# Optimization experiments

Hardware: AMD Instinct MI355X
Metric: run time of the kernel (lower is better)

## Reference

```python
import jax, jax.numpy as jnp
import numpy as np

D_MODEL = 1024
N_HEADS = 16
HEAD_DIM = D_MODEL // N_HEADS


def setup_inputs() -> dict:
    key = jax.random.key(0)
    k_x, k_wqkv, k_bqkv, k_wo, k_bo = jax.random.split(key, 5)
    b, t = 4, 2048
    s = 1.0 / np.sqrt(D_MODEL)
    return {
        "x": jax.random.normal(k_x, (b, t, D_MODEL), dtype=jnp.float32),
        "w_qkv": jax.random.uniform(k_wqkv, (D_MODEL, 3 * D_MODEL), jnp.float32, -s, s),
        "b_qkv": jax.random.uniform(k_bqkv, (3 * D_MODEL,), jnp.float32, -s, s),
        "w_out": jax.random.uniform(k_wo, (D_MODEL, D_MODEL), jnp.float32, -s, s),
        "b_out": jax.random.uniform(k_bo, (D_MODEL,), jnp.float32, -s, s),
    }


def reference(x, w_qkv, b_qkv, w_out, b_out):
    b, t, _ = x.shape
    # fused QKV projection -> [b, t, 3, h, d] -> q,k,v each [b, h, t, d]
    qkv = (x @ w_qkv + b_qkv).reshape(b, t, 3, N_HEADS, HEAD_DIM)
    q, k, v = jnp.moveaxis(qkv, 2, 0)          # each [b, t, h, d]
    q = q.transpose(0, 2, 1, 3)                # [b, h, t, d]
    k = k.transpose(0, 2, 1, 3)
    v = v.transpose(0, 2, 1, 3)
    scale = 1.0 / np.sqrt(HEAD_DIM).astype(np.float32)
    logits = jnp.einsum('bhqd,bhkd->bhqk', q, k) * scale
    causal = jnp.tril(jnp.ones((t, t), dtype=bool))
    logits = jnp.where(causal, logits, jnp.finfo(logits.dtype).min)
    attn = jax.nn.softmax(logits, axis=-1)
    out = jnp.einsum('bhqk,bhkd->bhqd', attn, v)      # [b, h, t, d]
    out = out.transpose(0, 2, 1, 3).reshape(b, t, D_MODEL)
    return out @ w_out + b_out
```

## Files before the change

### kernel.cpp

```cpp
#include <hip/hip_runtime.h>
#include <hip/hip_bf16.h>
#include <math.h>

#define NHEADS 16
#define HDIM   64
#define SEQT   2048
#define NBATCH 4
#define DMODEL 1024
#define MROWS  (NBATCH * SEQT)

typedef __bf16 bf16;
typedef bf16  bf16x8 __attribute__((ext_vector_type(8)));
typedef float f32x4  __attribute__((ext_vector_type(4)));
typedef float f32x16 __attribute__((ext_vector_type(16)));
typedef unsigned int u32x4 __attribute__((ext_vector_type(4)));

#define MFMA_BF16(a, b, c) __builtin_amdgcn_mfma_f32_16x16x32_bf16((a), (b), (c), 0, 0, 0)
#define MFMA32(a, b, c)    __builtin_amdgcn_mfma_f32_32x32x16_bf16((a), (b), (c), 0, 0, 0)
#define Z16 {0.f,0.f,0.f,0.f,0.f,0.f,0.f,0.f,0.f,0.f,0.f,0.f,0.f,0.f,0.f,0.f}
#define LOG2E 1.44269504f

__device__ __forceinline__ void gload_lds16(const void* g, void* l) {
  __builtin_amdgcn_global_load_lds((const __attribute__((address_space(1))) void*)g,
                                   (__attribute__((address_space(3))) void*)l, 16, 0, 0);
}

__device__ __forceinline__ unsigned cvtpk_bf16(float lo, float hi) {
  unsigned r;
  asm("v_cvt_pk_bf16_f32 %0, %1, %2" : "=v"(r) : "v"(lo), "v"(hi));
  return r;
}
__device__ __forceinline__ void plswap(unsigned& a, unsigned& b) {
  asm volatile("v_permlane32_swap_b32 %0, %1" : "+v"(a), "+v"(b));
}
__device__ __forceinline__ float exp2v(float x) {
  float r;
  asm("v_exp_f32 %0, %1" : "=v"(r) : "v"(x));
  return r;
}


__global__ __launch_bounds__(256) void k_cvt_f32_bf16(const float* __restrict__ in,
                                                      bf16* __restrict__ out, int n8) {
  int i = blockIdx.x * blockDim.x + threadIdx.x;
  if (i >= n8) return;
  const float4* in4 = (const float4*)in;
  float4 a = in4[(size_t)i * 2], b = in4[(size_t)i * 2 + 1];
  bf16x8 v;
  v[0] = (bf16)a.x; v[1] = (bf16)a.y; v[2] = (bf16)a.z; v[3] = (bf16)a.w;
  v[4] = (bf16)b.x; v[5] = (bf16)b.y; v[6] = (bf16)b.z; v[7] = (bf16)b.w;
  *(bf16x8*)(out + (size_t)i * 8) = v;
}

__global__ __launch_bounds__(256) void k_transpose_f32_bf16(const float* __restrict__ in,
                                                            bf16* __restrict__ out,
                                                            int R, int C) {
  int nct = C >> 6;
  int rt = blockIdx.x / nct, ct = blockIdx.x % nct;
  __shared__ float tile[64][65];
  int tid = threadIdx.x;
#pragma unroll
  for (int i = 0; i < 16; i++) {
    int e = i * 256 + tid, r = e >> 6, c = e & 63;
    tile[r][c] = in[(size_t)(rt * 64 + r) * C + ct * 64 + c];
  }
  __syncthreads();
#pragma unroll
  for (int i = 0; i < 16; i++) {
    int e = i * 256 + tid, r = e >> 6, c = e & 63;
    out[(size_t)(ct * 64 + r) * R + rt * 64 + c] = (bf16)tile[c][r];
  }
}

__global__ __launch_bounds__(256) void k_transpose_v(const bf16* __restrict__ v,
                                                     bf16* __restrict__ vt) {
  int tt = blockIdx.x & 31;
  int bh = blockIdx.x >> 5;
  __shared__ bf16 tile[64][65];
  int tid = threadIdx.x;
  const bf16* src = v + (size_t)bh * SEQT * 64 + (size_t)tt * 64 * 64;
#pragma unroll
  for (int i = 0; i < 16; i++) {
    int e = i * 256 + tid, r = e >> 6, c = e & 63;
    tile[r][c] = src[r * 64 + c];
  }
  __syncthreads();
  bf16* dst = vt + (size_t)bh * 64 * SEQT + tt * 64;
#pragma unroll
  for (int i = 0; i < 16; i++) {
    int e = i * 256 + tid, r = e >> 6, c = e & 63;
    dst[(size_t)r * SEQT + c] = tile[c][r];
  }
}


__device__ __forceinline__ void gemm128_core(const bf16* __restrict__ A,
                                             const bf16* __restrict__ Bt,
                                             int K, int bm, int bn, char* smem,
                                             f32x4 (&acc)[4][4]) {
  int tid = threadIdx.x, lane = tid & 63, w = tid >> 6;
  int l15 = lane & 15, g = lane >> 4;
  int wrow = (w >> 1) * 64, wcol = (w & 1) * 64;
  char* As = smem;
  char* Bs = smem + 8192;
  const char* Ag = (const char*)(A + (size_t)bm * 128 * K);
  const char* Bg = (const char*)(Bt + (size_t)bn * 128 * K);
  const int rowB = K * 2;
  int srow = w * 16 + (lane >> 2);
  int scol = (lane & 3) * 16;

  for (int kt = 0; kt < K / 32; kt++) {
#pragma unroll
    for (int is = 0; is < 2; is++) {
      int row = is * 64 + srow;
      gload_lds16(Ag + (size_t)row * rowB + kt * 64 + scol, As + is * 4096 + w * 1024);
      gload_lds16(Bg + (size_t)row * rowB + kt * 64 + scol, Bs + is * 4096 + w * 1024);
    }
    __syncthreads();
    bf16x8 af[4], bfr[4];
#pragma unroll
    for (int i = 0; i < 4; i++)
      af[i] = *(const bf16x8*)&As[(wrow + i * 16 + l15) * 64 + g * 16];
#pragma unroll
    for (int j = 0; j < 4; j++)
      bfr[j] = *(const bf16x8*)&Bs[(wcol + j * 16 + l15) * 64 + g * 16];
    __builtin_amdgcn_s_setprio(1);
#pragma unroll
    for (int i = 0; i < 4; i++)
#pragma unroll
      for (int j = 0; j < 4; j++)
        acc[i][j] = MFMA_BF16(af[i], bfr[j], acc[i][j]);
    __builtin_amdgcn_s_setprio(0);
    __syncthreads();
  }
}

__global__ __launch_bounds__(256) void k_gemm_qkv(const bf16* __restrict__ A,
                                                  const bf16* __restrict__ Bt,
                                                  const float* __restrict__ bias,
                                                  bf16* __restrict__ Qo,
                                                  bf16* __restrict__ Ko,
                                                  bf16* __restrict__ Vo) {
  const int K = DMODEL, NB = 24;
  int bid = (blockIdx.x & 7) * 192 + (blockIdx.x >> 3);
  int bm = bid / NB, bn = bid % NB;
  __shared__ __align__(16) char smem[16384];
  f32x4 acc[4][4] = {};
  gemm128_core(A, Bt, K, bm, bn, smem, acc);

  int tid = threadIdx.x, lane = tid & 63, w = tid >> 6;
  int l15 = lane & 15, g = lane >> 4;
  int wrow = (w >> 1) * 64, wcol = (w & 1) * 64;
  int rowbase = bm * 128 + wrow;
  int b = (bm * 128) >> 11;
#pragma unroll
  for (int j = 0; j < 4; j++) {
    int n = bn * 128 + wcol + j * 16 + l15;
    float bj = bias[n];
    int which = n >> 10;
    int nn = n & 1023;
    int head = nn >> 6, d = nn & 63;
    bf16* dst = (which == 0) ? Qo : (which == 1) ? Ko : Vo;
    size_t base = ((size_t)(b * NHEADS + head) * SEQT) * 64 + d;
#pragma unroll
    for (int i = 0; i < 4; i++) {
#pragma unroll
      for (int r = 0; r < 4; r++) {
        int row = rowbase + i * 16 + g * 4 + r;
        int t = row & (SEQT - 1);
        dst[base + (size_t)t * 64] = (bf16)(acc[i][j][r] + bj);
      }
    }
  }
}

__global__ __launch_bounds__(256) void k_gemm_out(const bf16* __restrict__ A,
                                                  const bf16* __restrict__ Bt,
                                                  const float* __restrict__ bias,
                                                  float* __restrict__ C) {
  const int K = DMODEL, NB = 8;
  int bid = (blockIdx.x & 7) * 64 + (blockIdx.x >> 3);
  int bm = bid / NB, bn = bid % NB;
  __shared__ __align__(16) char smem[16384];
  f32x4 acc[4][4] = {};
  gemm128_core(A, Bt, K, bm, bn, smem, acc);

  int tid = threadIdx.x, lane = tid & 63, w = tid >> 6;
  int l15 = lane & 15, g = lane >> 4;
  int wrow = (w >> 1) * 64, wcol = (w & 1) * 64;
#pragma unroll
  for (int j = 0; j < 4; j++) {
    int n = bn * 128 + wcol + j * 16 + l15;
    float bj = bias[n];
#pragma unroll
    for (int i = 0; i < 4; i++) {
#pragma unroll
      for (int r = 0; r < 4; r++) {
        int row = bm * 128 + wrow + i * 16 + g * 4 + r;
        C[(size_t)row * DMODEL + n] = acc[i][j][r] + bj;
      }
    }
  }
}


__global__ __launch_bounds__(128) void k_attn(const bf16* __restrict__ Q,
                                              const bf16* __restrict__ Kg,
                                              const bf16* __restrict__ VT,
                                              bf16* __restrict__ Oo) {
  int bh = blockIdx.x & 63;
  int qi = 31 - (blockIdx.x >> 6);
  int tid = threadIdx.x, lane = tid & 63, wv = tid >> 6;
  int l31 = lane & 31, hi = lane >> 5;
  __shared__ __align__(16) char smem[32768];

  const bf16* Qbh = Q + (size_t)bh * SEQT * 64;
  const char* Kbyte = (const char*)(Kg + (size_t)bh * SEQT * 64);
  const char* Vbyte = (const char*)(VT + (size_t)bh * 64 * SEQT);
  int qbase = qi * 64 + wv * 32;
  int ql = qbase + l31;

  int pp[4], lgK[4]; size_t vOff[4];
#pragma unroll
  for (int c = 0; c < 4; c++) {
    int p = c * 2048 + tid * 16;
    int row = p >> 7;
    int lg = p ^ ((row & 7) << 4);
    pp[c] = p; lgK[c] = lg;
    vOff[c] = (size_t)row * (SEQT * 2) + (lg & 127);
  }

  bf16x8 qf[4];
#pragma unroll
  for (int s = 0; s < 4; s++) {
    bf16x8 v = *(const bf16x8*)(Qbh + (size_t)ql * 64 + s * 16 + hi * 8);
#pragma unroll
    for (int e = 0; e < 8; e++) v[e] = (bf16)((float)v[e] * 0.125f);
    qf[s] = v;
  }

  bf16x8 onesf;
#pragma unroll
  for (int e = 0; e < 8; e++) onesf[e] = (bf16)1.0f;

  float m = -INFINITY;
  f32x16 o0 = Z16, o1 = Z16, lacc = Z16;

#pragma unroll
  for (int c = 0; c < 4; c++) {
    gload_lds16(Kbyte + lgK[c], smem + pp[c]);
    gload_lds16(Vbyte + vOff[c], smem + 16384 + pp[c]);
  }

  int NT = qi + 1;
  for (int t = 0; t < NT; t++) {
    __syncthreads();
    if (t + 1 < NT) {
      int nx = (t + 1) & 1;
      const char* kg = Kbyte + (size_t)(t + 1) * 8192;
      const char* vg = Vbyte + (size_t)(t + 1) * 128;
#pragma unroll
      for (int c = 0; c < 4; c++) {
        gload_lds16(kg + lgK[c], smem + nx * 8192 + pp[c]);
        gload_lds16(vg + vOff[c], smem + 16384 + nx * 8192 + pp[c]);
      }
    }
    const char* Ks = smem + (t & 1) * 8192;
    const char* Vs = smem + 16384 + (t & 1) * 8192;

    f32x16 st[2];
    __builtin_amdgcn_s_setprio(1);
#pragma unroll
    for (int h = 0; h < 2; h++) {
      f32x16 acc = Z16;
#pragma unroll
      for (int s = 0; s < 4; s++) {
        int row = h * 32 + l31;
        bf16x8 kf = *(const bf16x8*)&Ks[(row * 128 + s * 32 + hi * 16) ^ ((l31 & 7) << 4)];
        acc = MFMA32(kf, qf[s], acc);
      }
      st[h] = acc;
    }
    __builtin_amdgcn_s_setprio(0);

    if (t == NT - 1) {
      int rel = ql - (t * 64 + 4 * hi);
#pragma unroll
      for (int r = 0; r < 16; r++) {
        const int R0 = (r & 3) + 8 * (r >> 2);
        if (R0 > rel) st[0][r] = -INFINITY;
        if (R0 > rel - 32) st[1][r] = -INFINITY;
      }
    }

    float m0 = -INFINITY, m1 = -INFINITY, m2 = -INFINITY, m3 = -INFINITY;
#pragma unroll
    for (int h = 0; h < 2; h++)
#pragma unroll
      for (int r = 0; r < 16; r += 4) {
        m0 = fmaxf(m0, st[h][r]);
        m1 = fmaxf(m1, st[h][r + 1]);
        m2 = fmaxf(m2, st[h][r + 2]);
        m3 = fmaxf(m3, st[h][r + 3]);
      }
    float mx = fmaxf(fmaxf(m0, m1), fmaxf(m2, m3));
    mx = fmaxf(mx, __shfl_xor(mx, 32));

    if (__any(mx > m + 8.f)) {
      float mn = fmaxf(m, mx);
      float co = exp2v((m - mn) * LOG2E);
      m = mn;
#pragma unroll
      for (int r = 0; r < 16; r++) {
        const int R0 = (r & 3) + 8 * (r >> 2);
        float fac = __shfl(co, R0 + 4 * hi);
        o0[r] *= fac; o1[r] *= fac; lacc[r] *= fac;
      }
    }

    float negmq = -m * LOG2E;
#pragma unroll
    for (int h = 0; h < 2; h++)
#pragma unroll
      for (int r = 0; r < 16; r++)
        st[h][r] = exp2v(fmaf(st[h][r], LOG2E, negmq));

    __builtin_amdgcn_s_setprio(1);
#pragma unroll
    for (int h = 0; h < 2; h++) {
      unsigned pw[8];
#pragma unroll
      for (int i = 0; i < 8; i++) pw[i] = cvtpk_bf16(st[h][2 * i], st[h][2 * i + 1]);
      plswap(pw[0], pw[2]); plswap(pw[1], pw[3]);
      plswap(pw[4], pw[6]); plswap(pw[5], pw[7]);
      u32x4 f0 = {pw[0], pw[1], pw[2], pw[3]};
      u32x4 f1 = {pw[4], pw[5], pw[6], pw[7]};
      bf16x8 pa0 = __builtin_bit_cast(bf16x8, f0);
      bf16x8 pa1 = __builtin_bit_cast(bf16x8, f1);
      lacc = MFMA32(pa0, onesf, lacc);
      lacc = MFMA32(pa1, onesf, lacc);
      {
        int vrow = l31;
        bf16x8 bv0 = *(const bf16x8*)&Vs[(vrow * 128 + (2 * h) * 32 + hi * 16) ^ ((l31 & 7) << 4)];
        bf16x8 bv1 = *(const bf16x8*)&Vs[(vrow * 128 + (2 * h + 1) * 32 + hi * 16) ^ ((l31 & 7) << 4)];
        o0 = MFMA32(pa0, bv0, o0);
        o0 = MFMA32(pa1, bv1, o0);
      }
      {
        int vrow = 32 + l31;
        bf16x8 bv0 = *(const bf16x8*)&Vs[(vrow * 128 + (2 * h) * 32 + hi * 16) ^ ((l31 & 7) << 4)];
        bf16x8 bv1 = *(const bf16x8*)&Vs[(vrow * 128 + (2 * h + 1) * 32 + hi * 16) ^ ((l31 & 7) << 4)];
        o1 = MFMA32(pa0, bv0, o1);
        o1 = MFMA32(pa1, bv1, o1);
      }
    }
    __builtin_amdgcn_s_setprio(0);
  }

  int b = bh >> 4, hd = bh & 15;
#pragma unroll
  for (int r = 0; r < 16; r++) {
    const int R0 = (r & 3) + 8 * (r >> 2);
    int qrow = qbase + R0 + 4 * hi;
    float inv = 1.f / lacc[r];
    size_t off = ((size_t)(b * SEQT + qrow)) * DMODEL + hd * 64;
    Oo[off + l31]      = (bf16)(o0[r] * inv);
    Oo[off + 32 + l31] = (bf16)(o1[r] * inv);
  }
}


extern "C" void kernel_launch(void* const* d_in, const int* in_sizes, int n_in,
                              void* d_out, int out_size, void* d_ws, size_t ws_size,
                              hipStream_t stream) {
  const float* x     = (const float*)d_in[0];
  const float* w_qkv = (const float*)d_in[1];
  const float* b_qkv = (const float*)d_in[2];
  const float* w_out = (const float*)d_in[3];
  const float* b_out = (const float*)d_in[4];
  float* out = (float*)d_out;

  char* ws = (char*)d_ws;
  bf16* xb    = (bf16*)(ws);
  bf16* wqkvT = (bf16*)(ws + (16u << 20));
  bf16* woutT = (bf16*)(ws + (22u << 20));
  bf16* Qb    = (bf16*)(ws + (24u << 20));
  bf16* Kb    = (bf16*)(ws + (40u << 20));
  bf16* Vb    = (bf16*)(ws + (56u << 20));
  bf16* VTb   = (bf16*)(ws + (72u << 20));
  bf16* attn_o = xb;

  k_cvt_f32_bf16<<<(MROWS * DMODEL / 8 + 255) / 256, 256, 0, stream>>>(x, xb, MROWS * DMODEL / 8);
  k_transpose_f32_bf16<<<16 * 48, 256, 0, stream>>>(w_qkv, wqkvT, DMODEL, 3 * DMODEL);
  k_transpose_f32_bf16<<<16 * 16, 256, 0, stream>>>(w_out, woutT, DMODEL, DMODEL);
  k_gemm_qkv<<<64 * 24, 256, 0, stream>>>(xb, wqkvT, b_qkv, Qb, Kb, Vb);
  k_transpose_v<<<64 * 32, 256, 0, stream>>>(Vb, VTb);
  k_attn<<<32 * 64, 128, 0, stream>>>(Qb, Kb, VTb, attn_o);
  k_gemm_out<<<64 * 8, 256, 0, stream>>>(attn_o, woutT, b_out, out);
}
```

Before: 268.7 us.

## Rewrite projection GEMMs with 4-stage LDS pipeline, swizzle, and 128x256 tiles

Replaces the single-buffered 128x128 GEMM core with a 512-thread, 128x256-tile core. It uses a 4-deep ring of LDS buffers, prefetches three k-steps ahead with explicit vmcnt waits, and XOR-swizzles LDS addresses to avoid bank conflicts. The goal is to hide global-load latency and raise operand reuse in both the QKV and output projections. In exchange it needs 96KB of LDS per block, which limits occupancy, and it drops the L2-friendly block-index remapping.

Result: no change. 267.6 us (-0.4%).

```diff
diff --git a/kernel.cpp b/kernel.cpp
--- a/kernel.cpp
+++ b/kernel.cpp
@@ -94,109 +94,131 @@
 }
 
 
-__device__ __forceinline__ void gemm128_core(const bf16* __restrict__ A,
+__device__ __forceinline__ void stage_tile(const char* Ag, const char* Bg,
+                                           char* buf, int kt, int tid) {
+  int pa = tid * 16;
+  int ra = pa >> 6, ca = pa & 63;
+  gload_lds16(Ag + (size_t)ra * 2048 + kt * 64 + (ca ^ ((ra & 3) << 4)), buf + pa);
+  int pb0 = tid * 16;
+  int rb0 = pb0 >> 6, cb0 = pb0 & 63;
+  gload_lds16(Bg + (size_t)rb0 * 2048 + kt * 64 + (cb0 ^ ((rb0 & 3) << 4)),
+              buf + 8192 + pb0);
+  int pb1 = pb0 + 8192;
+  int rb1 = pb1 >> 6, cb1 = pb1 & 63;
+  gload_lds16(Bg + (size_t)rb1 * 2048 + kt * 64 + (cb1 ^ ((rb1 & 3) << 4)),
+              buf + 8192 + pb1);
+}
+
+__device__ __forceinline__ void gemm_core512(const bf16* __restrict__ A,
                                              const bf16* __restrict__ Bt,
-                                             int K, int bm, int bn, char* smem,
+                                             int bm, int bn, char* smem,
                                              f32x4 (&acc)[4][4]) {
-  int tid = threadIdx.x, lane = tid & 63, w = tid >> 6;
+  const int NK = 32;
+  int tid = threadIdx.x, lane = tid & 63;
   int l15 = lane & 15, g = lane >> 4;
-  int wrow = (w >> 1) * 64, wcol = (w & 1) * 64;
-  char* As = smem;
-  char* Bs = smem + 8192;
-  const char* Ag = (const char*)(A + (size_t)bm * 128 * K);
-  const char* Bg = (const char*)(Bt + (size_t)bn * 128 * K);
-  const int rowB = K * 2;
-  int srow = w * 16 + (lane >> 2);
-  int scol = (lane & 3) * 16;
-
-  for (int kt = 0; kt < K / 32; kt++) {
-#pragma unroll
-    for (int is = 0; is < 2; is++) {
-      int row = is * 64 + srow;
-      gload_lds16(Ag + (size_t)row * rowB + kt * 64 + scol, As + is * 4096 + w * 1024);
-      gload_lds16(Bg + (size_t)row * rowB + kt * 64 + scol, Bs + is * 4096 + w * 1024);
-    }
-    __syncthreads();
-    bf16x8 af[4], bfr[4];
+  int wid = tid >> 6, wr = wid >> 2, wc = wid & 3;
+  const char* Ag = (const char*)(A + (size_t)bm * 128 * 1024);
+  const char* Bg = (const char*)(Bt + (size_t)bn * 256 * 1024);
+
+  int aoff[4], boff[4];
+#pragma unroll
+  for (int i = 0; i < 4; i++) {
+    int row = wr * 64 + i * 16 + l15;
+    aoff[i] = row * 64 + ((g * 16) ^ ((row & 3) << 4));
+  }
+#pragma unroll
+  for (int j = 0; j < 4; j++) {
+    int row = wc * 64 + j * 16 + l15;
+    boff[j] = 8192 + row * 64 + ((g * 16) ^ ((row & 3) << 4));
+  }
+
+  stage_tile(Ag, Bg, smem + 0 * 24576, 0, tid);
+  stage_tile(Ag, Bg, smem + 1 * 24576, 1, tid);
+  stage_tile(Ag, Bg, smem + 2 * 24576, 2, tid);
+
+#pragma unroll 1
+  for (int kt = 0; kt < NK; ++kt) {
+    if (kt + 3 < NK) stage_tile(Ag, Bg, smem + ((kt + 3) & 3) * 24576, kt + 3, tid);
+    int ahead = NK - 1 - kt;
+    if (ahead >= 3)      asm volatile("s_waitcnt vmcnt(9)" ::: "memory");
+    else if (ahead == 2) asm volatile("s_waitcnt vmcnt(6)" ::: "memory");
+    else if (ahead == 1) asm volatile("s_waitcnt vmcnt(3)" ::: "memory");
+    else                 asm volatile("s_waitcnt vmcnt(0)" ::: "memory");
+    __builtin_amdgcn_s_barrier();
+    const char* buf = smem + (kt & 3) * 24576;
+    bf16x8 af[4], bq[4];
+#pragma unroll
+    for (int i = 0; i < 4; i++) af[i] = *(const bf16x8*)(buf + aoff[i]);
+#pragma unroll
+    for (int j = 0; j < 4; j++) bq[j] = *(const bf16x8*)(buf + boff[j]);
+    asm volatile("s_waitcnt lgkmcnt(0)" ::: "memory");
+    __builtin_amdgcn_s_barrier();
 #pragma unroll
     for (int i = 0; i < 4; i++)
-      af[i] = *(const bf16x8*)&As[(wrow + i * 16 + l15) * 64 + g * 16];
-#pragma unroll
-    for (int j = 0; j < 4; j++)
-      bfr[j] = *(const bf16x8*)&Bs[(wcol + j * 16 + l15) * 64 + g * 16];
-    __builtin_amdgcn_s_setprio(1);
-#pragma unroll
-    for (int i = 0; i < 4; i++)
 #pragma unroll
       for (int j = 0; j < 4; j++)
-        acc[i][j] = MFMA_BF16(af[i], bfr[j], acc[i][j]);
-    __builtin_amdgcn_s_setprio(0);
-    __syncthreads();
-  }
-}
-
-__global__ __launch_bounds__(256) void k_gemm_qkv(const bf16* __restrict__ A,
+        acc[i][j] = MFMA_BF16(af[i], bq[j], acc[i][j]);
+  }
+}
+
+__global__ __launch_bounds__(512) void k_gemm_qkv(const bf16* __restrict__ A,
                                                   const bf16* __restrict__ Bt,
                                                   const float* __restrict__ bias,
                                                   bf16* __restrict__ Qo,
                                                   bf16* __restrict__ Ko,
                                                   bf16* __restrict__ Vo) {
-  const int K = DMODEL, NB = 24;
-  int bid = (blockIdx.x & 7) * 192 + (blockIdx.x >> 3);
-  int bm = bid / NB, bn = bid % NB;
-  __shared__ __align__(16) char smem[16384];
+  const int NB = 12;
+  int bm = blockIdx.x / NB, bn = blockIdx.x % NB;
+  __shared__ __align__(16) char smem[98304];
   f32x4 acc[4][4] = {};
-  gemm128_core(A, Bt, K, bm, bn, smem, acc);
-
-  int tid = threadIdx.x, lane = tid & 63, w = tid >> 6;
+  gemm_core512(A, Bt, bm, bn, smem, acc);
+
+  int tid = threadIdx.x, lane = tid & 63;
   int l15 = lane & 15, g = lane >> 4;
-  int wrow = (w >> 1) * 64, wcol = (w & 1) * 64;
-  int rowbase = bm * 128 + wrow;
-  int b = (bm * 128) >> 11;
+  int wid = tid >> 6, wr = wid >> 2, wc = wid & 3;
 #pragma unroll
   for (int j = 0; j < 4; j++) {
-    int n = bn * 128 + wcol + j * 16 + l15;
+    int n = bn * 256 + wc * 64 + j * 16 + l15;
     float bj = bias[n];
     int which = n >> 10;
     int nn = n & 1023;
     int head = nn >> 6, d = nn & 63;
     bf16* dst = (which == 0) ? Qo : (which == 1) ? Ko : Vo;
-    size_t base = ((size_t)(b * NHEADS + head) * SEQT) * 64 + d;
 #pragma unroll
     for (int i = 0; i < 4; i++) {
 #pragma unroll
       for (int r = 0; r < 4; r++) {
-        int row = rowbase + i * 16 + g * 4 + r;
-        int t = row & (SEQT - 1);
-        dst[base + (size_t)t * 64] = (bf16)(acc[i][j][r] + bj);
-      }
-    }
-  }
-}
-
-__global__ __launch_bounds__(256) void k_gemm_out(const bf16* __restrict__ A,
+        int row = bm * 128 + wr * 64 + i * 16 + g * 4 + r;
+        int b = row >> 11, t = row & (SEQT - 1);
+        dst[((size_t)(b * NHEADS + head) * SEQT + t) * 64 + d] =
+            (bf16)(acc[i][j][r] + bj);
+      }
+    }
+  }
+}
+
+__global__ __launch_bounds__(512) void k_gemm_out(const bf16* __restrict__ A,
                                                   const bf16* __restrict__ Bt,
                                                   const float* __restrict__ bias,
                                                   float* __restrict__ C) {
-  const int K = DMODEL, NB = 8;
-  int bid = (blockIdx.x & 7) * 64 + (blockIdx.x >> 3);
-  int bm = bid / NB, bn = bid % NB;
-  __shared__ __align__(16) char smem[16384];
+  const int NB = 4;
+  int bm = blockIdx.x / NB, bn = blockIdx.x % NB;
+  __shared__ __align__(16) char smem[98304];
   f32x4 acc[4][4] = {};
-  gemm128_core(A, Bt, K, bm, bn, smem, acc);
-
-  int tid = threadIdx.x, lane = tid & 63, w = tid >> 6;
+  gemm_core512(A, Bt, bm, bn, smem, acc);
+
+  int tid = threadIdx.x, lane = tid & 63;
   int l15 = lane & 15, g = lane >> 4;
-  int wrow = (w >> 1) * 64, wcol = (w & 1) * 64;
+  int wid = tid >> 6, wr = wid >> 2, wc = wid & 3;
 #pragma unroll
   for (int j = 0; j < 4; j++) {
-    int n = bn * 128 + wcol + j * 16 + l15;
+    int n = bn * 256 + wc * 64 + j * 16 + l15;
     float bj = bias[n];
 #pragma unroll
     for (int i = 0; i < 4; i++) {
 #pragma unroll
       for (int r = 0; r < 4; r++) {
-        int row = bm * 128 + wrow + i * 16 + g * 4 + r;
+        int row = bm * 128 + wr * 64 + i * 16 + g * 4 + r;
         C[(size_t)row * DMODEL + n] = acc[i][j][r] + bj;
       }
     }
@@ -393,8 +415,8 @@
   k_cvt_f32_bf16<<<(MROWS * DMODEL / 8 + 255) / 256, 256, 0, stream>>>(x, xb, MROWS * DMODEL / 8);
   k_transpose_f32_bf16<<<16 * 48, 256, 0, stream>>>(w_qkv, wqkvT, DMODEL, 3 * DMODEL);
   k_transpose_f32_bf16<<<16 * 16, 256, 0, stream>>>(w_out, woutT, DMODEL, DMODEL);
-  k_gemm_qkv<<<64 * 24, 256, 0, stream>>>(xb, wqkvT, b_qkv, Qb, Kb, Vb);
+  k_gemm_qkv<<<768, 512, 0, stream>>>(xb, wqkvT, b_qkv, Qb, Kb, Vb);
   k_transpose_v<<<64 * 32, 256, 0, stream>>>(Vb, VTb);
   k_attn<<<32 * 64, 128, 0, stream>>>(Qb, Kb, VTb, attn_o);
-  k_gemm_out<<<64 * 8, 256, 0, stream>>>(attn_o, woutT, b_out, out);
-}
+  k_gemm_out<<<256, 512, 0, stream>>>(attn_o, woutT, b_out, out);
+}
```
